# Optimization experiments

Hardware: AMD Instinct MI355X
Metric: run time of the kernel (lower is better)

Reference implementation:

```python
import jax, jax.numpy as jnp
import numpy as np

N = 50000      # num nodes
E = 400000     # num edges
D = 384        # input_dim
H = 4          # heads
C = 128        # hidden_dim per head
HC = H * C     # 512


def setup_inputs() -> dict:
    key = jax.random.key(0)
    ks = jax.random.split(key, 32)
    w = lambda k, shape: jax.random.normal(k, shape, jnp.float32) * 0.05
    inp = {
        "x": jax.random.normal(ks[0], (N, D), jnp.float32),
        "edge_index": jax.random.randint(ks[1], (2, E), 0, N, dtype=jnp.int32),
    }
    dims = [(D, HC), (HC, HC)]  # layer0 in=384, layer1 in=512
    i = 2
    for l, (din, dout) in enumerate(dims):
        for nm in ["q", "k", "v", "s"]:  # query/key/value/skip linears
            inp[f"{nm}{l}_w"] = w(ks[i], (dout, din)); i += 1
            inp[f"{nm}{l}_b"] = jnp.zeros((dout,), jnp.float32)
    inp["out_w"] = w(ks[i], (D, HC))
    inp["out_b"] = jnp.zeros((D,), jnp.float32)
    return inp


def _transformer_conv(x, src, dst, Wq, bq, Wk, bk, Wv, bv, Ws, bs):
    # PyG TransformerConv, concat=True, root_weight=True, no edge features.
    n = x.shape[0]
    q = (x @ Wq.T + bq).reshape(n, H, C)
    k = (x @ Wk.T + bk).reshape(n, H, C)
    v = (x @ Wv.T + bv).reshape(n, H, C)
    # per-edge attention logits [E, H]; target = dst, source = src
    alpha = (q[dst] * k[src]).sum(-1) / jnp.sqrt(jnp.float32(C))
    m = jax.ops.segment_max(alpha, dst, num_segments=n)
    m = jnp.where(jnp.isfinite(m), m, 0.0)  # nodes with no in-edges
    e = jnp.exp(alpha - m[dst])
    denom = jax.ops.segment_sum(e, dst, num_segments=n)
    a = e / (denom[dst] + 1e-16)             # segment softmax [E, H]
    msg = v[src] * a[:, :, None]             # [E, H, C]
    agg = jax.ops.segment_sum(msg, dst, num_segments=n).reshape(n, HC)
    return agg + x @ Ws.T + bs               # + root/skip connection


def reference(x, edge_index,
              q0_w, q0_b, k0_w, k0_b, v0_w, v0_b, s0_w, s0_b,
              q1_w, q1_b, k1_w, k1_b, v1_w, v1_b, s1_w, s1_b,
              out_w, out_b):
    src, dst = edge_index[0], edge_index[1]
    h = _transformer_conv(x, src, dst, q0_w, q0_b, k0_w, k0_b, v0_w, v0_b, s0_w, s0_b)
    h = jax.nn.relu(h)
    h = _transformer_conv(h, src, dst, q1_w, q1_b, k1_w, k1_b, v1_w, v1_b, s1_w, s1_b)
    h = jax.nn.relu(h)
    return h @ out_w.T + out_b  # [N, D]
```

## Files before the change

### kernel.cpp

```cpp
#include <hip/hip_runtime.h>
#include <hip/hip_bf16.h>

#define NN 50000
#define NE 400000
#define DD 384
#define HC 512

typedef unsigned int u32;
typedef unsigned short u16;
typedef __attribute__((ext_vector_type(8))) short bf16x8;
typedef __attribute__((ext_vector_type(4))) float f32x4;

#define AS1 __attribute__((address_space(1)))
#define AS3 __attribute__((address_space(3)))

__device__ __forceinline__ float bflo(u32 u){ return __uint_as_float(u << 16); }
__device__ __forceinline__ float bfhi(u32 u){ return __uint_as_float(u & 0xFFFF0000u); }
__device__ __forceinline__ u16 f2bf(float f){
    u32 u = __float_as_uint(f);
    return (u16)((u + 0x7FFFu + ((u >> 16) & 1u)) >> 16);
}
__device__ __forceinline__ u32 pack2(float a, float b){
    return (u32)f2bf(a) | ((u32)f2bf(b) << 16);
}
__device__ __forceinline__ float dot8(const float* q, uint4 k){
    return q[0] * bflo(k.x) + q[1] * bfhi(k.x)
         + q[2] * bflo(k.y) + q[3] * bfhi(k.y)
         + q[4] * bflo(k.z) + q[5] * bfhi(k.z)
         + q[6] * bflo(k.w) + q[7] * bfhi(k.w);
}

template<int K>
__global__ __launch_bounds__(512)
void gemm_ws(const u16* __restrict__ Ab, const u16* __restrict__ Wb,
             const float* __restrict__ bias,
             u16* __restrict__ oQ, u16* __restrict__ oK,
             u16* __restrict__ oV, u16* __restrict__ oS)
{
    constexpr int NKT  = K / 64;
    constexpr int WCH  = K / 8;
    constexpr int NPAN = (NN + 127) / 128;
    __shared__ char smW[128 * K * 2];
    __shared__ char smA[2][16384];

    const int b   = blockIdx.x;
    const int xcd = b & 7;
    const int idx = b >> 3;
    const int ct  = idx & 15;
    const int rh  = idx >> 4;

    const int tid  = threadIdx.x;
    const int lane = tid & 63;
    const int w    = tid >> 6;
    const int wq   = w >> 1;
    const int wc   = w & 1;
    const int r16  = lane & 15;
    const int kq   = lane >> 4;

    const u16* Wrow0 = Wb + (size_t)ct * 128 * K;
    #pragma unroll
    for (int p = 0; p < (128 * WCH) / 512; ++p) {
        int ci = p * 512 + tid;
        int row = ci / WCH, pc = ci % WCH;
        int lc = (pc & ~7) | ((pc ^ row) & 7);
        __builtin_amdgcn_global_load_lds((const AS1 u32*)(Wrow0 + (size_t)row * K + lc * 8),
                                         (AS3 u32*)(smW + (size_t)ci * 16), 16, 0, 0);
    }

    auto panel = [&](int j) { return (2 * j + rh) * 8 + xcd; };
    int np = 0;
    while (panel(np) < NPAN) ++np;
    const int total = np * NKT;

    auto stageA = [&](int t) {
        int j = t / NKT, kc = t - (t / NKT) * NKT;
        int m0 = panel(j) * 128;
        #pragma unroll
        for (int p = 0; p < 2; ++p) {
            int ci = p * 512 + tid;
            int row = ci >> 3, pc = ci & 7;
            int lc = pc ^ (row & 7);
            int gr = m0 + row; if (gr >= NN) gr = NN - 1;
            __builtin_amdgcn_global_load_lds((const AS1 u32*)(Ab + (size_t)gr * K + kc * 64 + lc * 8),
                                             (AS3 u32*)(smA[t & 1] + ci * 16), 16, 0, 0);
        }
    };

    stageA(0);
    stageA(1);

    f32x4 acc[2][4] = {};

    const int qsel = ct >> 2;
    u16* outp = (qsel == 0) ? oQ : (qsel == 1) ? oK : (qsel == 2) ? oV : oS;
    const int cb = (ct & 3) * 128 + wc * 64;
    float bv4[4];
    #pragma unroll
    for (int ni = 0; ni < 4; ++ni) bv4[ni] = bias[ct * 128 + wc * 64 + ni * 16 + r16];

    for (int t = 0; t < total; ++t) {
        if (t + 1 < total) { asm volatile("s_waitcnt vmcnt(2)" ::: "memory"); }
        else               { asm volatile("s_waitcnt vmcnt(0)" ::: "memory"); }
        __builtin_amdgcn_s_barrier();
        __builtin_amdgcn_sched_barrier(0);

        const int jj = t / NKT;
        const int kt = t - jj * NKT;
        const char* bufA = smA[t & 1];
        #pragma unroll
        for (int kk = 0; kk < 2; ++kk) {
            bf16x8 av[2], bv[4];
            #pragma unroll
            for (int i = 0; i < 2; ++i) {
                int rowA = wq * 32 + i * 16 + r16;
                int c = kk * 4 + kq;
                av[i] = *(const bf16x8*)(bufA + rowA * 128 + ((c ^ (rowA & 7)) << 4));
            }
            #pragma unroll
            for (int i = 0; i < 4; ++i) {
                int rowW = wc * 64 + i * 16 + r16;
                int c = kt * 8 + kk * 4 + kq;
                int pcw = (c & ~7) | ((c ^ rowW) & 7);
                bv[i] = *(const bf16x8*)(smW + (size_t)rowW * (K * 2) + (pcw << 4));
            }
            #pragma unroll
            for (int mi = 0; mi < 2; ++mi)
                #pragma unroll
                for (int ni = 0; ni < 4; ++ni)
                    acc[mi][ni] = __builtin_amdgcn_mfma_f32_16x16x32_bf16(
                        av[mi], bv[ni], acc[mi][ni], 0, 0, 0);
        }

        __builtin_amdgcn_sched_barrier(0);
        __builtin_amdgcn_s_barrier();
        __builtin_amdgcn_sched_barrier(0);

        if (kt == NKT - 1) {
            int m0 = panel(jj) * 128;
            #pragma unroll
            for (int ni = 0; ni < 4; ++ni) {
                int col = cb + ni * 16 + r16;
                float bb = bv4[ni];
                #pragma unroll
                for (int mi = 0; mi < 2; ++mi)
                    #pragma unroll
                    for (int r = 0; r < 4; ++r) {
                        int gr = m0 + wq * 32 + mi * 16 + kq * 4 + r;
                        if (gr < NN) outp[(size_t)gr * 512 + col] = f2bf(acc[mi][ni][r] + bb);
                        acc[mi][ni][r] = 0.f;
                    }
            }
        }
        if (t + 2 < total) stageA(t + 2);
    }
}

__global__ __launch_bounds__(512)
void gemm_ws_f(const u16* __restrict__ Ab, const u16* __restrict__ Wb,
               const float* __restrict__ bias, float* __restrict__ oF)
{
    constexpr int K    = 512;
    constexpr int NKT  = 8;
    constexpr int WCH  = 64;
    constexpr int NPAN = (NN + 127) / 128;
    __shared__ char smW[128 * K * 2];
    __shared__ char smA[2][16384];

    const int b   = blockIdx.x;
    const int xcd = b & 7;
    const int idx = b >> 3;
    const int ct  = idx % 3;
    const int rh  = idx / 3;

    const int tid  = threadIdx.x;
    const int lane = tid & 63;
    const int w    = tid >> 6;
    const int wq   = w >> 1;
    const int wc   = w & 1;
    const int r16  = lane & 15;
    const int kq   = lane >> 4;

    const u16* Wrow0 = Wb + (size_t)ct * 128 * K;
    #pragma unroll
    for (int p = 0; p < (128 * WCH) / 512; ++p) {
        int ci = p * 512 + tid;
        int row = ci / WCH, pc = ci % WCH;
        int lc = (pc & ~7) | ((pc ^ row) & 7);
        __builtin_amdgcn_global_load_lds((const AS1 u32*)(Wrow0 + (size_t)row * K + lc * 8),
                                         (AS3 u32*)(smW + (size_t)ci * 16), 16, 0, 0);
    }

    auto panel = [&](int j) { return (10 * j + rh) * 8 + xcd; };
    int np = 0;
    while (panel(np) < NPAN) ++np;
    const int total = np * NKT;

    auto stageA = [&](int t) {
        int j = t / NKT, kc = t - (t / NKT) * NKT;
        int m0 = panel(j) * 128;
        #pragma unroll
        for (int p = 0; p < 2; ++p) {
            int ci = p * 512 + tid;
            int row = ci >> 3, pc = ci & 7;
            int lc = pc ^ (row & 7);
            int gr = m0 + row; if (gr >= NN) gr = NN - 1;
            __builtin_amdgcn_global_load_lds((const AS1 u32*)(Ab + (size_t)gr * K + kc * 64 + lc * 8),
                                             (AS3 u32*)(smA[t & 1] + ci * 16), 16, 0, 0);
        }
    };

    stageA(0);
    stageA(1);

    f32x4 acc[2][4] = {};

    const int cb = ct * 128 + wc * 64;
    float bv4[4];
    #pragma unroll
    for (int ni = 0; ni < 4; ++ni) bv4[ni] = bias[cb + ni * 16 + r16];

    for (int t = 0; t < total; ++t) {
        if (t + 1 < total) { asm volatile("s_waitcnt vmcnt(2)" ::: "memory"); }
        else               { asm volatile("s_waitcnt vmcnt(0)" ::: "memory"); }
        __builtin_amdgcn_s_barrier();
        __builtin_amdgcn_sched_barrier(0);

        const int jj = t / NKT;
        const int kt = t - jj * NKT;
        const char* bufA = smA[t & 1];
        #pragma unroll
        for (int kk = 0; kk < 2; ++kk) {
            bf16x8 av[2], bv[4];
            #pragma unroll
            for (int i = 0; i < 2; ++i) {
                int rowA = wq * 32 + i * 16 + r16;
                int c = kk * 4 + kq;
                av[i] = *(const bf16x8*)(bufA + rowA * 128 + ((c ^ (rowA & 7)) << 4));
            }
            #pragma unroll
            for (int i = 0; i < 4; ++i) {
                int rowW = wc * 64 + i * 16 + r16;
                int c = kt * 8 + kk * 4 + kq;
                int pcw = (c & ~7) | ((c ^ rowW) & 7);
                bv[i] = *(const bf16x8*)(smW + (size_t)rowW * (K * 2) + (pcw << 4));
            }
            #pragma unroll
            for (int mi = 0; mi < 2; ++mi)
                #pragma unroll
                for (int ni = 0; ni < 4; ++ni)
                    acc[mi][ni] = __builtin_amdgcn_mfma_f32_16x16x32_bf16(
                        av[mi], bv[ni], acc[mi][ni], 0, 0, 0);
        }

        __builtin_amdgcn_sched_barrier(0);
        __builtin_amdgcn_s_barrier();
        __builtin_amdgcn_sched_barrier(0);

        if (kt == NKT - 1) {
            int m0 = panel(jj) * 128;
            #pragma unroll
            for (int ni = 0; ni < 4; ++ni) {
                int col = cb + ni * 16 + r16;
                float bb = bv4[ni];
                #pragma unroll
                for (int mi = 0; mi < 2; ++mi)
                    #pragma unroll
                    for (int r = 0; r < 4; ++r) {
                        int gr = m0 + wq * 32 + mi * 16 + kq * 4 + r;
                        if (gr < NN) oF[(size_t)gr * 384 + col] = acc[mi][ni][r] + bb;
                        acc[mi][ni][r] = 0.f;
                    }
            }
        }
        if (t + 2 < total) stageA(t + 2);
    }
}

#define XG  2400000
#define W0G 24576
#define W1G 32768
#define WOG 24576
#define CVT_TOTAL (XG + 4*W0G + 4*W1G + WOG)

__global__ __launch_bounds__(256)
void cvt_all(const float* __restrict__ x,
             const float* q0w, const float* k0w, const float* v0w, const float* s0w,
             const float* q1w, const float* k1w, const float* v1w, const float* s1w,
             const float* ow,
             u16* __restrict__ Xb, u16* __restrict__ Wc0,
             u16* __restrict__ Wc1, u16* __restrict__ WcO)
{
    int i = blockIdx.x * 256 + threadIdx.x;
    if (i >= CVT_TOTAL) return;
    const float* s; u16* d; int g;
    if (i < XG) { s = x; d = Xb; g = i; }
    else {
        int j = i - XG;
        if (j < 4 * W0G) {
            int q = j / W0G; g = j - q * W0G;
            s = (q == 0 ? q0w : q == 1 ? k0w : q == 2 ? v0w : s0w);
            d = Wc0 + (size_t)q * W0G * 8;
        } else if ((j -= 4 * W0G) < 4 * W1G) {
            int q = j / W1G; g = j - q * W1G;
            s = (q == 0 ? q1w : q == 1 ? k1w : q == 2 ? v1w : s1w);
            d = Wc1 + (size_t)q * W1G * 8;
        } else { j -= 4 * W1G; s = ow; d = WcO; g = j; }
    }
    float4 f0 = ((const float4*)s)[(size_t)g * 2];
    float4 f1 = ((const float4*)s)[(size_t)g * 2 + 1];
    uint4 o;
    o.x = pack2(f0.x, f0.y); o.y = pack2(f0.z, f0.w);
    o.z = pack2(f1.x, f1.y); o.w = pack2(f1.z, f1.w);
    ((uint4*)d)[g] = o;
}

__global__ __launch_bounds__(256)
void pack_bias(const float* q0, const float* k0, const float* v0, const float* s0,
               const float* q1, const float* k1, const float* v1, const float* s1,
               const float* ob, float* __restrict__ dst)
{
    int i = blockIdx.x * 256 + threadIdx.x;
    if (i >= 4480) return;
    float v;
    if (i < 2048) {
        int j = i & 511, q = i >> 9;
        v = (q == 0 ? q0 : q == 1 ? k0 : q == 2 ? v0 : s0)[j];
    } else if (i < 4096) {
        int j = i - 2048; int q = j >> 9; j &= 511;
        v = (q == 0 ? q1 : q == 1 ? k1 : q == 2 ? v1 : s1)[j];
    } else {
        v = ob[i - 4096];
    }
    dst[i] = v;
}

__global__ __launch_bounds__(256)
void zero_deg(int* __restrict__ deg)
{
    int i = blockIdx.x * 256 + threadIdx.x;
    if (i < NN) deg[i] = 0;
}

__global__ __launch_bounds__(256)
void hist_dst(const int* __restrict__ dst, int* __restrict__ deg)
{
    int e = blockIdx.x * 256 + threadIdx.x;
    if (e < NE) atomicAdd(&deg[dst[e]], 1);
}

__global__ __launch_bounds__(1024)
void scan_deg(const int* __restrict__ deg, int* __restrict__ rowptr,
              int* __restrict__ cursor)
{
    __shared__ int wsum[16];
    const int tid = threadIdx.x, lane = tid & 63, wid = tid >> 6;
    int carry = 0;
    for (int base = 0; base < NN; base += 4096) {
        int idx = base + tid * 4;
        int4 v4 = make_int4(0, 0, 0, 0);
        if (idx + 3 < NN)      v4 = *(const int4*)(deg + idx);
        else if (idx < NN) {
            v4.x = deg[idx];
            if (idx + 1 < NN) v4.y = deg[idx + 1];
            if (idx + 2 < NN) v4.z = deg[idx + 2];
        }
        int t0 = v4.x, t1 = t0 + v4.y, t2 = t1 + v4.z, t3 = t2 + v4.w;
        int v = t3;
        #pragma unroll
        for (int off = 1; off < 64; off <<= 1) {
            int t = __shfl_up(v, off, 64);
            if (lane >= off) v += t;
        }
        if (lane == 63) wsum[wid] = v;
        __syncthreads();
        if (wid == 0) {
            int s = (lane < 16) ? wsum[lane] : 0;
            #pragma unroll
            for (int off = 1; off < 16; off <<= 1) {
                int t = __shfl_up(s, off, 16);
                if ((lane & 15) >= off) s += t;
            }
            if (lane < 16) wsum[lane] = s;
        }
        __syncthreads();
        int woff  = (wid == 0) ? 0 : wsum[wid - 1];
        int total = wsum[15];
        int texcl = carry + woff + (v - t3);
        if (idx < NN)     { rowptr[idx]     = texcl;      cursor[idx]     = texcl; }
        if (idx + 1 < NN) { rowptr[idx + 1] = texcl + t0; cursor[idx + 1] = texcl + t0; }
        if (idx + 2 < NN) { rowptr[idx + 2] = texcl + t1; cursor[idx + 2] = texcl + t1; }
        if (idx + 3 < NN) { rowptr[idx + 3] = texcl + t2; cursor[idx + 3] = texcl + t2; }
        carry += total;
        __syncthreads();
    }
    if (tid == 0) rowptr[NN] = NE;
}

__global__ __launch_bounds__(256)
void scatter_edges(const int* __restrict__ src, const int* __restrict__ dst,
                   int* __restrict__ cursor, int* __restrict__ esrc_ord)
{
    int e = blockIdx.x * 256 + threadIdx.x;
    if (e >= NE) return;
    int pos = atomicAdd(&cursor[dst[e]], 1);
    esrc_ord[pos] = src[e];
}

__global__ __launch_bounds__(256)
void node_attn(const u16* __restrict__ Qb, const u16* __restrict__ Kb,
               const u16* __restrict__ Vb, const int* __restrict__ rowptr,
               const int* __restrict__ esrc, const u16* __restrict__ skipb,
               u16* __restrict__ outb)
{
    int d = blockIdx.x * 4 + (threadIdx.x >> 6);
    if (d >= NN) return;
    int lane = threadIdx.x & 63;

    uint4 qv = *((const uint4*)(Qb + (size_t)d * HC) + lane);
    float q[8] = { bflo(qv.x), bfhi(qv.x), bflo(qv.y), bfhi(qv.y),
                   bflo(qv.z), bfhi(qv.z), bflo(qv.w), bfhi(qv.w) };

    int beg = rowptr[d], end = rowptr[d + 1];
    int cnt = end - beg;
    float m = -INFINITY, den = 0.f;
    float acc[8] = {};

    uint4 k0, v0, k1, v1;
    if (cnt > 0) {
        int s = esrc[beg];
        k0 = *((const uint4*)(Kb + (size_t)s * HC) + lane);
        v0 = *((const uint4*)(Vb + (size_t)s * HC) + lane);
    }
    if (cnt > 1) {
        int s = esrc[beg + 1];
        k1 = *((const uint4*)(Kb + (size_t)s * HC) + lane);
        v1 = *((const uint4*)(Vb + (size_t)s * HC) + lane);
    }

    int i = beg;
    for (; i + 1 < end; i += 2) {
        uint4 ka = k0, va = v0, kb = k1, vb = v1;
        if (i + 2 < end) {
            int s = esrc[i + 2];
            k0 = *((const uint4*)(Kb + (size_t)s * HC) + lane);
            v0 = *((const uint4*)(Vb + (size_t)s * HC) + lane);
        }
        if (i + 3 < end) {
            int s = esrc[i + 3];
            k1 = *((const uint4*)(Kb + (size_t)s * HC) + lane);
            v1 = *((const uint4*)(Vb + (size_t)s * HC) + lane);
        }
        float s0 = dot8(q, ka);
        float s1 = dot8(q, kb);
        #pragma unroll
        for (int off = 1; off < 16; off <<= 1) {
            s0 += __shfl_xor(s0, off, 64);
            s1 += __shfl_xor(s1, off, 64);
        }
        float a0 = s0 * 0.08838834764831845f;
        float a1 = s1 * 0.08838834764831845f;

        float mnew  = fmaxf(m, fmaxf(a0, a1));
        float scale = __expf(m - mnew);
        float p0    = __expf(a0 - mnew);
        float p1    = __expf(a1 - mnew);
        den = den * scale + p0 + p1;

        acc[0] = acc[0] * scale + p0 * bflo(va.x) + p1 * bflo(vb.x);
        acc[1] = acc[1] * scale + p0 * bfhi(va.x) + p1 * bfhi(vb.x);
        acc[2] = acc[2] * scale + p0 * bflo(va.y) + p1 * bflo(vb.y);
        acc[3] = acc[3] * scale + p0 * bfhi(va.y) + p1 * bfhi(vb.y);
        acc[4] = acc[4] * scale + p0 * bflo(va.z) + p1 * bflo(vb.z);
        acc[5] = acc[5] * scale + p0 * bfhi(va.z) + p1 * bfhi(vb.z);
        acc[6] = acc[6] * scale + p0 * bflo(va.w) + p1 * bflo(vb.w);
        acc[7] = acc[7] * scale + p0 * bfhi(va.w) + p1 * bfhi(vb.w);
        m = mnew;
    }
    if (i < end) {
        float s0 = dot8(q, k0);
        #pragma unroll
        for (int off = 1; off < 16; off <<= 1) s0 += __shfl_xor(s0, off, 64);
        float a0 = s0 * 0.08838834764831845f;
        float mnew  = fmaxf(m, a0);
        float scale = __expf(m - mnew);
        float p0    = __expf(a0 - mnew);
        den = den * scale + p0;
        acc[0] = acc[0] * scale + p0 * bflo(v0.x);
        acc[1] = acc[1] * scale + p0 * bfhi(v0.x);
        acc[2] = acc[2] * scale + p0 * bflo(v0.y);
        acc[3] = acc[3] * scale + p0 * bfhi(v0.y);
        acc[4] = acc[4] * scale + p0 * bflo(v0.z);
        acc[5] = acc[5] * scale + p0 * bfhi(v0.z);
        acc[6] = acc[6] * scale + p0 * bflo(v0.w);
        acc[7] = acc[7] * scale + p0 * bfhi(v0.w);
    }

    float inv = 1.f / (den + 1e-16f);
    size_t base = (size_t)d * HC + lane * 8;
    uint4 sv = *((const uint4*)(skipb + base));
    float sk[8] = { bflo(sv.x), bfhi(sv.x), bflo(sv.y), bfhi(sv.y),
                    bflo(sv.z), bfhi(sv.z), bflo(sv.w), bfhi(sv.w) };
    uint4 o;
    o.x = pack2(fmaxf(acc[0] * inv + sk[0], 0.f), fmaxf(acc[1] * inv + sk[1], 0.f));
    o.y = pack2(fmaxf(acc[2] * inv + sk[2], 0.f), fmaxf(acc[3] * inv + sk[3], 0.f));
    o.z = pack2(fmaxf(acc[4] * inv + sk[4], 0.f), fmaxf(acc[5] * inv + sk[5], 0.f));
    o.w = pack2(fmaxf(acc[6] * inv + sk[6], 0.f), fmaxf(acc[7] * inv + sk[7], 0.f));
    *(uint4*)(outb + base) = o;
}

extern "C" void kernel_launch(void* const* d_in, const int* in_sizes, int n_in,
                              void* d_out, int out_size, void* d_ws, size_t ws_size,
                              hipStream_t stream)
{
    const float* x   = (const float*)d_in[0];
    const int* ei    = (const int*)d_in[1];
    const int* esrc  = ei;
    const int* edst  = ei + NE;
    const float* q0w = (const float*)d_in[2];  const float* q0b = (const float*)d_in[3];
    const float* k0w = (const float*)d_in[4];  const float* k0b = (const float*)d_in[5];
    const float* v0w = (const float*)d_in[6];  const float* v0b = (const float*)d_in[7];
    const float* s0w = (const float*)d_in[8];  const float* s0b = (const float*)d_in[9];
    const float* q1w = (const float*)d_in[10]; const float* q1b = (const float*)d_in[11];
    const float* k1w = (const float*)d_in[12]; const float* k1b = (const float*)d_in[13];
    const float* v1w = (const float*)d_in[14]; const float* v1b = (const float*)d_in[15];
    const float* s1w = (const float*)d_in[16]; const float* s1b = (const float*)d_in[17];
    const float* ow  = (const float*)d_in[18]; const float* obs = (const float*)d_in[19];

    char* p = (char*)d_ws;
    auto take = [&](size_t bytes) { void* r = (void*)p; p += (bytes + 255) & ~(size_t)255; return r; };
    u16*   Qb     = (u16*)take((size_t)NN * HC * 2);
    u16*   Vb     = (u16*)take((size_t)NN * HC * 2);
    u16*   Hb     = (u16*)take((size_t)NN * HC * 2);
    u16*   Sb     = (u16*)take((size_t)NN * HC * 2);
    u16*   Xb     = (u16*)take((size_t)NN * DD * 2);
    u16*   Wc0    = (u16*)take((size_t)2048 * DD * 2);
    u16*   Wc1    = (u16*)take((size_t)2048 * HC * 2);
    u16*   WcO    = (u16*)take((size_t)DD * HC * 2);
    float* barena = (float*)take(4480 * 4);

    char* dob = (char*)d_out;
    u16* Kb       = (u16*)dob;
    int* deg      = (int*)(dob + 51200000);
    int* rowptr   = (int*)(dob + 51400192);
    int* cursor   = (int*)(dob + 51600384);
    int* esrc_ord = (int*)(dob + 51800576);

    dim3 blk(256);
    int gN   = (NN + 255) / 256;
    int gE   = (NE + 255) / 256;
    int gnod = (NN + 3) / 4;

    pack_bias<<<(4480 + 255) / 256, blk, 0, stream>>>(q0b, k0b, v0b, s0b,
                                                      q1b, k1b, v1b, s1b, obs, barena);
    cvt_all<<<(CVT_TOTAL + 255) / 256, blk, 0, stream>>>(x,
        q0w, k0w, v0w, s0w, q1w, k1w, v1w, s1w, ow, Xb, Wc0, Wc1, WcO);

    zero_deg      <<<gN, blk, 0, stream>>>(deg);
    hist_dst      <<<gE, blk, 0, stream>>>(edst, deg);
    scan_deg      <<<1, 1024, 0, stream>>>(deg, rowptr, cursor);
    scatter_edges <<<gE, blk, 0, stream>>>(esrc, edst, cursor, esrc_ord);

    gemm_ws<DD><<<256, 512, 0, stream>>>(Xb, Wc0, barena, Qb, Kb, Vb, Sb);
    node_attn<<<gnod, blk, 0, stream>>>(Qb, Kb, Vb, rowptr, esrc_ord, Sb, Hb);

    gemm_ws<HC><<<256, 512, 0, stream>>>(Hb, Wc1, barena + 2048, Qb, Kb, Vb, Sb);
    node_attn<<<gnod, blk, 0, stream>>>(Qb, Kb, Vb, rowptr, esrc_ord, Sb, Hb);

    gemm_ws_f<<<240, 512, 0, stream>>>(Hb, WcO, barena + 4096, (float*)d_out);
}
```

Before: 673.2 us.

## Unroll attention gather to four edges and merge prep kernels

The per-node attention loop now processes four edges per iteration instead of two, keeping four K/V rows in flight. V prefetches are issued after the accumulation so fewer registers stay live at once. The bias-pack kernel is folded into the conversion kernel, and the degree-zeroing kernel is replaced by a memset, which removes two kernel launches. The deeper prefetch raises register pressure and may lower occupancy in the gather-bound attention kernel.

```diff
diff --git a/kernel.cpp b/kernel.cpp
--- a/kernel.cpp
+++ b/kernel.cpp
@@ -281,17 +281,37 @@
 #define W1G 32768
 #define WOG 24576
 #define CVT_TOTAL (XG + 4*W0G + 4*W1G + WOG)
+#define PREP_TOTAL (CVT_TOTAL + 4480)
 
 __global__ __launch_bounds__(256)
-void cvt_all(const float* __restrict__ x,
-             const float* q0w, const float* k0w, const float* v0w, const float* s0w,
-             const float* q1w, const float* k1w, const float* v1w, const float* s1w,
-             const float* ow,
-             u16* __restrict__ Xb, u16* __restrict__ Wc0,
-             u16* __restrict__ Wc1, u16* __restrict__ WcO)
+void prep_all(const float* __restrict__ x,
+              const float* q0w, const float* k0w, const float* v0w, const float* s0w,
+              const float* q1w, const float* k1w, const float* v1w, const float* s1w,
+              const float* ow,
+              const float* q0b, const float* k0b, const float* v0b, const float* s0b,
+              const float* q1b, const float* k1b, const float* v1b, const float* s1b,
+              const float* ob,
+              u16* __restrict__ Xb, u16* __restrict__ Wc0,
+              u16* __restrict__ Wc1, u16* __restrict__ WcO,
+              float* __restrict__ barena)
 {
     int i = blockIdx.x * 256 + threadIdx.x;
-    if (i >= CVT_TOTAL) return;
+    if (i >= PREP_TOTAL) return;
+    if (i >= CVT_TOTAL) {
+        int t = i - CVT_TOTAL;
+        float v;
+        if (t < 2048) {
+            int j = t & 511, q = t >> 9;
+            v = (q == 0 ? q0b : q == 1 ? k0b : q == 2 ? v0b : s0b)[j];
+        } else if (t < 4096) {
+            int j = t - 2048; int q = j >> 9; j &= 511;
+            v = (q == 0 ? q1b : q == 1 ? k1b : q == 2 ? v1b : s1b)[j];
+        } else {
+            v = ob[t - 4096];
+        }
+        barena[t] = v;
+        return;
+    }
     const float* s; u16* d; int g;
     if (i < XG) { s = x; d = Xb; g = i; }
     else {
@@ -315,33 +335,6 @@
 }
 
 __global__ __launch_bounds__(256)
-void pack_bias(const float* q0, const float* k0, const float* v0, const float* s0,
-               const float* q1, const float* k1, const float* v1, const float* s1,
-               const float* ob, float* __restrict__ dst)
-{
-    int i = blockIdx.x * 256 + threadIdx.x;
-    if (i >= 4480) return;
-    float v;
-    if (i < 2048) {
-        int j = i & 511, q = i >> 9;
-        v = (q == 0 ? q0 : q == 1 ? k0 : q == 2 ? v0 : s0)[j];
-    } else if (i < 4096) {
-        int j = i - 2048; int q = j >> 9; j &= 511;
-        v = (q == 0 ? q1 : q == 1 ? k1 : q == 2 ? v1 : s1)[j];
-    } else {
-        v = ob[i - 4096];
-    }
-    dst[i] = v;
-}
-
-__global__ __launch_bounds__(256)
-void zero_deg(int* __restrict__ deg)
-{
-    int i = blockIdx.x * 256 + threadIdx.x;
-    if (i < NN) deg[i] = 0;
-}
-
-__global__ __launch_bounds__(256)
 void hist_dst(const int* __restrict__ dst, int* __restrict__ deg)
 {
     int e = blockIdx.x * 256 + threadIdx.x;
@@ -421,79 +414,89 @@
                    bflo(qv.z), bfhi(qv.z), bflo(qv.w), bfhi(qv.w) };
 
     int beg = rowptr[d], end = rowptr[d + 1];
-    int cnt = end - beg;
+    int n = end - beg;
     float m = -INFINITY, den = 0.f;
     float acc[8] = {};
 
-    uint4 k0, v0, k1, v1;
-    if (cnt > 0) {
-        int s = esrc[beg];
-        k0 = *((const uint4*)(Kb + (size_t)s * HC) + lane);
-        v0 = *((const uint4*)(Vb + (size_t)s * HC) + lane);
-    }
-    if (cnt > 1) {
-        int s = esrc[beg + 1];
-        k1 = *((const uint4*)(Kb + (size_t)s * HC) + lane);
-        v1 = *((const uint4*)(Vb + (size_t)s * HC) + lane);
-    }
+    uint4 k0, k1, k2, k3, v0, v1, v2, v3;
+    if (n > 0){ int s = esrc[beg];     k0 = *((const uint4*)(Kb + (size_t)s * HC) + lane);
+                                       v0 = *((const uint4*)(Vb + (size_t)s * HC) + lane); }
+    if (n > 1){ int s = esrc[beg + 1]; k1 = *((const uint4*)(Kb + (size_t)s * HC) + lane);
+                                       v1 = *((const uint4*)(Vb + (size_t)s * HC) + lane); }
+    if (n > 2){ int s = esrc[beg + 2]; k2 = *((const uint4*)(Kb + (size_t)s * HC) + lane);
+                                       v2 = *((const uint4*)(Vb + (size_t)s * HC) + lane); }
+    if (n > 3){ int s = esrc[beg + 3]; k3 = *((const uint4*)(Kb + (size_t)s * HC) + lane);
+                                       v3 = *((const uint4*)(Vb + (size_t)s * HC) + lane); }
+
+    auto single = [&](uint4 kk, uint4 vv){
+        float s0 = dot8(q, kk);
+        #pragma unroll
+        for (int off = 1; off < 16; off <<= 1) s0 += __shfl_xor(s0, off, 64);
+        float a0 = s0 * 0.08838834764831845f;
+        float mnew = fmaxf(m, a0);
+        float sc = __expf(m - mnew);
+        float p0 = __expf(a0 - mnew);
+        den = den * sc + p0;
+        acc[0] = acc[0] * sc + p0 * bflo(vv.x);
+        acc[1] = acc[1] * sc + p0 * bfhi(vv.x);
+        acc[2] = acc[2] * sc + p0 * bflo(vv.y);
+        acc[3] = acc[3] * sc + p0 * bfhi(vv.y);
+        acc[4] = acc[4] * sc + p0 * bflo(vv.z);
+        acc[5] = acc[5] * sc + p0 * bfhi(vv.z);
+        acc[6] = acc[6] * sc + p0 * bflo(vv.w);
+        acc[7] = acc[7] * sc + p0 * bfhi(vv.w);
+        m = mnew;
+    };
 
     int i = beg;
-    for (; i + 1 < end; i += 2) {
-        uint4 ka = k0, va = v0, kb = k1, vb = v1;
-        if (i + 2 < end) {
-            int s = esrc[i + 2];
-            k0 = *((const uint4*)(Kb + (size_t)s * HC) + lane);
-            v0 = *((const uint4*)(Vb + (size_t)s * HC) + lane);
-        }
-        if (i + 3 < end) {
-            int s = esrc[i + 3];
-            k1 = *((const uint4*)(Kb + (size_t)s * HC) + lane);
-            v1 = *((const uint4*)(Vb + (size_t)s * HC) + lane);
-        }
-        float s0 = dot8(q, ka);
-        float s1 = dot8(q, kb);
+    for (; i + 3 < end; i += 4) {
+        float s0 = dot8(q, k0), s1 = dot8(q, k1), s2 = dot8(q, k2), s3 = dot8(q, k3);
+        bool h0 = i + 4 < end, h1 = i + 5 < end, h2 = i + 6 < end, h3 = i + 7 < end;
+        int sn0 = 0, sn1 = 0, sn2 = 0, sn3 = 0;
+        if (h0) sn0 = esrc[i + 4];
+        if (h1) sn1 = esrc[i + 5];
+        if (h2) sn2 = esrc[i + 6];
+        if (h3) sn3 = esrc[i + 7];
+        if (h0) k0 = *((const uint4*)(Kb + (size_t)sn0 * HC) + lane);
+        if (h1) k1 = *((const uint4*)(Kb + (size_t)sn1 * HC) + lane);
+        if (h2) k2 = *((const uint4*)(Kb + (size_t)sn2 * HC) + lane);
+        if (h3) k3 = *((const uint4*)(Kb + (size_t)sn3 * HC) + lane);
         #pragma unroll
         for (int off = 1; off < 16; off <<= 1) {
             s0 += __shfl_xor(s0, off, 64);
             s1 += __shfl_xor(s1, off, 64);
+            s2 += __shfl_xor(s2, off, 64);
+            s3 += __shfl_xor(s3, off, 64);
         }
         float a0 = s0 * 0.08838834764831845f;
         float a1 = s1 * 0.08838834764831845f;
-
-        float mnew  = fmaxf(m, fmaxf(a0, a1));
-        float scale = __expf(m - mnew);
-        float p0    = __expf(a0 - mnew);
-        float p1    = __expf(a1 - mnew);
-        den = den * scale + p0 + p1;
-
-        acc[0] = acc[0] * scale + p0 * bflo(va.x) + p1 * bflo(vb.x);
-        acc[1] = acc[1] * scale + p0 * bfhi(va.x) + p1 * bfhi(vb.x);
-        acc[2] = acc[2] * scale + p0 * bflo(va.y) + p1 * bflo(vb.y);
-        acc[3] = acc[3] * scale + p0 * bfhi(va.y) + p1 * bfhi(vb.y);
-        acc[4] = acc[4] * scale + p0 * bflo(va.z) + p1 * bflo(vb.z);
-        acc[5] = acc[5] * scale + p0 * bfhi(va.z) + p1 * bfhi(vb.z);
-        acc[6] = acc[6] * scale + p0 * bflo(va.w) + p1 * bflo(vb.w);
-        acc[7] = acc[7] * scale + p0 * bfhi(va.w) + p1 * bfhi(vb.w);
+        float a2 = s2 * 0.08838834764831845f;
+        float a3 = s3 * 0.08838834764831845f;
+
+        float mnew = fmaxf(fmaxf(fmaxf(a0, a1), fmaxf(a2, a3)), m);
+        float sc = __expf(m - mnew);
+        float p0 = __expf(a0 - mnew), p1 = __expf(a1 - mnew);
+        float p2 = __expf(a2 - mnew), p3 = __expf(a3 - mnew);
+        den = den * sc + ((p0 + p1) + (p2 + p3));
+
+        acc[0] = acc[0] * sc + p0 * bflo(v0.x) + p1 * bflo(v1.x) + p2 * bflo(v2.x) + p3 * bflo(v3.x);
+        acc[1] = acc[1] * sc + p0 * bfhi(v0.x) + p1 * bfhi(v1.x) + p2 * bfhi(v2.x) + p3 * bfhi(v3.x);
+        acc[2] = acc[2] * sc + p0 * bflo(v0.y) + p1 * bflo(v1.y) + p2 * bflo(v2.y) + p3 * bflo(v3.y);
+        acc[3] = acc[3] * sc + p0 * bfhi(v0.y) + p1 * bfhi(v1.y) + p2 * bfhi(v2.y) + p3 * bfhi(v3.y);
+        acc[4] = acc[4] * sc + p0 * bflo(v0.z) + p1 * bflo(v1.z) + p2 * bflo(v2.z) + p3 * bflo(v3.z);
+        acc[5] = acc[5] * sc + p0 * bfhi(v0.z) + p1 * bfhi(v1.z) + p2 * bfhi(v2.z) + p3 * bfhi(v3.z);
+        acc[6] = acc[6] * sc + p0 * bflo(v0.w) + p1 * bflo(v1.w) + p2 * bflo(v2.w) + p3 * bflo(v3.w);
+        acc[7] = acc[7] * sc + p0 * bfhi(v0.w) + p1 * bfhi(v1.w) + p2 * bfhi(v2.w) + p3 * bfhi(v3.w);
         m = mnew;
-    }
-    if (i < end) {
-        float s0 = dot8(q, k0);
-        #pragma unroll
-        for (int off = 1; off < 16; off <<= 1) s0 += __shfl_xor(s0, off, 64);
-        float a0 = s0 * 0.08838834764831845f;
-        float mnew  = fmaxf(m, a0);
-        float scale = __expf(m - mnew);
-        float p0    = __expf(a0 - mnew);
-        den = den * scale + p0;
-        acc[0] = acc[0] * scale + p0 * bflo(v0.x);
-        acc[1] = acc[1] * scale + p0 * bfhi(v0.x);
-        acc[2] = acc[2] * scale + p0 * bflo(v0.y);
-        acc[3] = acc[3] * scale + p0 * bfhi(v0.y);
-        acc[4] = acc[4] * scale + p0 * bflo(v0.z);
-        acc[5] = acc[5] * scale + p0 * bfhi(v0.z);
-        acc[6] = acc[6] * scale + p0 * bflo(v0.w);
-        acc[7] = acc[7] * scale + p0 * bfhi(v0.w);
-    }
+
+        if (h0) v0 = *((const uint4*)(Vb + (size_t)sn0 * HC) + lane);
+        if (h1) v1 = *((const uint4*)(Vb + (size_t)sn1 * HC) + lane);
+        if (h2) v2 = *((const uint4*)(Vb + (size_t)sn2 * HC) + lane);
+        if (h3) v3 = *((const uint4*)(Vb + (size_t)sn3 * HC) + lane);
+    }
+    if (i < end)     single(k0, v0);
+    if (i + 1 < end) single(k1, v1);
+    if (i + 2 < end) single(k2, v2);
 
     float inv = 1.f / (den + 1e-16f);
     size_t base = (size_t)d * HC + lane * 8;
@@ -546,16 +549,14 @@
     int* esrc_ord = (int*)(dob + 51800576);
 
     dim3 blk(256);
-    int gN   = (NN + 255) / 256;
     int gE   = (NE + 255) / 256;
     int gnod = (NN + 3) / 4;
 
-    pack_bias<<<(4480 + 255) / 256, blk, 0, stream>>>(q0b, k0b, v0b, s0b,
-                                                      q1b, k1b, v1b, s1b, obs, barena);
-    cvt_all<<<(CVT_TOTAL + 255) / 256, blk, 0, stream>>>(x,
-        q0w, k0w, v0w, s0w, q1w, k1w, v1w, s1w, ow, Xb, Wc0, Wc1, WcO);
-
-    zero_deg      <<<gN, blk, 0, stream>>>(deg);
+    prep_all<<<(PREP_TOTAL + 255) / 256, blk, 0, stream>>>(x,
+        q0w, k0w, v0w, s0w, q1w, k1w, v1w, s1w, ow,
+        q0b, k0b, v0b, s0b, q1b, k1b, v1b, s1b, obs,
+        Xb, Wc0, Wc1, WcO, barena);
+    hipMemsetAsync(deg, 0, (size_t)NN * 4, stream);
     hist_dst      <<<gE, blk, 0, stream>>>(edst, deg);
     scan_deg      <<<1, 1024, 0, stream>>>(deg, rowptr, cursor);
     scatter_edges <<<gE, blk, 0, stream>>>(esrc, edst, cursor, esrc_ord);
```

New measurement: 662.5 us. About the same (-1.6%).
